# Optimization experiments

Measured on AMD Instinct MI355X. Metric: run time of the kernel, lower is better.

Reference implementation:

```python
import jax, jax.numpy as jnp
import numpy as np

D_MODEL = 1024
NUM_HEAD = 16
D_HEAD = 64
SEQ = 1024
MEM = 1024
BATCH = 4
LN_EPS = 1e-5


def _rel_shift(x):
    # x: [i, j, b, n] -- Transformer-XL relative shift trick
    i, j, b, n = x.shape
    zero_pad = jnp.zeros((i, 1, b, n), dtype=x.dtype)
    x_padded = jnp.concatenate([zero_pad, x], axis=1).reshape(j + 1, i, b, n)
    return x_padded[1:].reshape(i, j, b, n)


def setup_inputs() -> dict:
    key = jax.random.key(0)
    ks = jax.random.split(key, 8)
    w_scale = 1.0 / np.sqrt(D_MODEL)  # keep activations O(1)
    total = MEM + SEQ
    return {
        "x": jax.random.normal(ks[0], (SEQ, BATCH, D_MODEL), jnp.float32),
        "memory": jax.random.normal(ks[1], (MEM, BATCH, D_MODEL), jnp.float32),
        "pos_emb": jax.random.normal(ks[2], (total, BATCH, D_MODEL), jnp.float32),
        "pos_bias_u": jax.random.normal(ks[3], (NUM_HEAD, D_HEAD), jnp.float32) * 0.02,
        "pos_bias_v": jax.random.normal(ks[4], (NUM_HEAD, D_HEAD), jnp.float32) * 0.02,
        "W_qkv": jax.random.normal(ks[5], (3 * NUM_HEAD * D_HEAD, D_MODEL), jnp.float32) * w_scale,
        "W_rel": jax.random.normal(ks[6], (NUM_HEAD * D_HEAD, D_MODEL), jnp.float32) * w_scale,
        "W_o": jax.random.normal(ks[7], (D_MODEL, NUM_HEAD * D_HEAD), jnp.float32) * w_scale,
        "ln_gamma": jnp.ones((D_MODEL,), jnp.float32),
        "ln_beta": jnp.zeros((D_MODEL,), jnp.float32),
    }


def reference(x, memory, pos_emb, pos_bias_u, pos_bias_v, W_qkv, W_rel, W_o, ln_gamma, ln_beta):
    seq_len = x.shape[0]
    c = jnp.concatenate([memory, x], axis=0)        # [T, B, D]
    T, B = c.shape[0], c.shape[1]
    n, d = pos_bias_u.shape
    scale = 1.0 / np.sqrt(d)

    heads = c @ W_qkv.T                              # [T, B, 3*n*d]
    q, k, v = jnp.split(heads, 3, axis=-1)
    q = q.reshape(T, B, n, d)[-seq_len:]             # [S, B, n, d]
    k = k.reshape(T, B, n, d)                        # [T, B, n, d]
    v = v.reshape(T, B, n, d)
    r = (pos_emb @ W_rel.T).reshape(T, B, n, d)      # [T, B, n, d]

    AC = jnp.einsum('ibnd,jbnd->ijbn', q + pos_bias_u, k)
    BD = _rel_shift(jnp.einsum('ibnd,jbnd->ijbn', q + pos_bias_v, r))
    attn_score = (AC + BD) * scale                   # [S, T, B, n]
    attn_prob = jax.nn.softmax(attn_score, axis=1)   # softmax over key dim (dropout = eval identity)

    attn_vec = jnp.einsum('ijbn,jbnd->ibnd', attn_prob, v).reshape(seq_len, B, n * d)
    attn_out = attn_vec @ W_o.T                      # [S, B, D]

    y = x + attn_out
    mu = jnp.mean(y, axis=-1, keepdims=True)
    var = jnp.mean(jnp.square(y - mu), axis=-1, keepdims=True)
    return ln_gamma * (y - mu) / jnp.sqrt(var + LN_EPS) + ln_beta
```

## Files before the change

kernel.cpp:

```cpp
#include <hip/hip_runtime.h>

#define S_ 1024
#define M_ 1024
#define T_ 2048
#define B_ 4
#define H_ 16
#define DM_ 1024
#define DH_ 64

typedef __attribute__((ext_vector_type(8))) short s16x8;
typedef __attribute__((ext_vector_type(16))) float f32x16;

__device__ __forceinline__ unsigned short f2b(float x){
  unsigned int u = __float_as_uint(x);
  u = (u + 0x7fffu + ((u>>16)&1u)) >> 16;
  return (unsigned short)u;
}
__device__ __forceinline__ float b2f(unsigned short h){
  return __uint_as_float(((unsigned int)h)<<16);
}
__device__ __forceinline__ uint4 pack8(const float* v){
  uint4 o;
  o.x = (unsigned)f2b(v[0]) | ((unsigned)f2b(v[1])<<16);
  o.y = (unsigned)f2b(v[2]) | ((unsigned)f2b(v[3])<<16);
  o.z = (unsigned)f2b(v[4]) | ((unsigned)f2b(v[5])<<16);
  o.w = (unsigned)f2b(v[6]) | ((unsigned)f2b(v[7])<<16);
  return o;
}
__device__ __forceinline__ void glds16(const unsigned short* g, unsigned short* l){
  __builtin_amdgcn_global_load_lds((const __attribute__((address_space(1))) void*)g,
                                   (__attribute__((address_space(3))) void*)l, 16, 0, 0);
}

#define BAR_L()  asm volatile("s_waitcnt lgkmcnt(0)\ns_barrier" ::: "memory")
#define BAR_VL() asm volatile("s_waitcnt vmcnt(0) lgkmcnt(0)\ns_barrier" ::: "memory")

__global__ __launch_bounds__(256) void cast_cat(const float* __restrict__ a,
    const float* __restrict__ b, unsigned short* __restrict__ dst, int n8, int na8)
{
  int i = blockIdx.x*256 + threadIdx.x;
  if (i >= n8) return;
  const float* src = (i < na8) ? (a + (size_t)i*8) : (b + ((size_t)(i-na8))*8);
  float4 x0 = *(const float4*)src;
  float4 x1 = *(const float4*)(src+4);
  float f[8] = {x0.x,x0.y,x0.z,x0.w,x1.x,x1.y,x1.z,x1.w};
  *(uint4*)&dst[(size_t)i*8] = pack8(f);
}

__global__ __launch_bounds__(256) void gemm_nt(const unsigned short* __restrict__ A,
    const unsigned short* __restrict__ Bw, void* __restrict__ Cout,
    const float* __restrict__ res, int Ntot, int K, int mode)
{
  __shared__ __align__(16) unsigned short a_s[128*64];
  __shared__ __align__(16) unsigned short b_s[128*64];
  const int tid = threadIdx.x;
  const int lane = tid & 63, wave = tid >> 6;
  const int wr = wave >> 1, wc = wave & 1;
  const long m0 = (long)blockIdx.y * 128, n0 = (long)blockIdx.x * 128;
  f32x16 acc[2][2];
  for (int qa=0;qa<2;qa++) for(int qb=0;qb<2;qb++) for (int e=0;e<16;e++) acc[qa][qb][e]=0.f;
  int srow[4], scol[4];
  for (int c = 0; c < 4; c++) {
    int ch = c*256 + tid;
    srow[c] = ch >> 3;
    scol[c] = (((ch & 7) ^ (srow[c] & 7))) * 8;
  }
  for (int k0 = 0; k0 < K; k0 += 64) {
    for (int c = 0; c < 4; c++) {
      int ch = c*256 + tid;
      glds16(&A[(size_t)(m0+srow[c])*K + k0 + scol[c]], &a_s[ch*8]);
      glds16(&Bw[(size_t)(n0+srow[c])*K + k0 + scol[c]], &b_s[ch*8]);
    }
    __syncthreads();
    for (int ks = 0; ks < 4; ks++) {
      const int kb = ks*2 + (lane>>5);
      s16x8 af[2], bf[2];
      for (int q = 0; q < 2; q++) {
        int ra = wr*64 + q*32 + (lane&31);
        int rb = wc*64 + q*32 + (lane&31);
        af[q] = *(const s16x8*)&a_s[ra*64 + ((kb ^ (ra&7))<<3)];
        bf[q] = *(const s16x8*)&b_s[rb*64 + ((kb ^ (rb&7))<<3)];
      }
      for (int qr=0;qr<2;qr++)
        for (int qc2=0;qc2<2;qc2++)
          acc[qr][qc2] = __builtin_amdgcn_mfma_f32_32x32x16_bf16(af[qr], bf[qc2], acc[qr][qc2], 0,0,0);
    }
    __syncthreads();
  }
  for (int qr=0;qr<2;qr++)
    for (int qc2=0;qc2<2;qc2++)
      for (int e=0;e<16;e++){
        long row = m0 + wr*64 + qr*32 + (e&3) + 8*(e>>2) + 4*(lane>>5);
        long col = n0 + wc*64 + qc2*32 + (lane&31);
        size_t o = (size_t)row*Ntot + col;
        if (mode == 0) ((unsigned short*)Cout)[o] = f2b(acc[qr][qc2][e]);
        else           ((float*)Cout)[o] = acc[qr][qc2][e] + res[o];
      }
}

__global__ __launch_bounds__(256) void scatter_quv(const unsigned short* __restrict__ qkvo,
   const float* __restrict__ u, const float* __restrict__ v,
   unsigned short* __restrict__ QU, unsigned short* __restrict__ QV)
{
  int gid = blockIdx.x*256 + threadIdx.x;
  int d0 = (gid & 7) * 8;
  int i  = (gid >> 3) & (S_-1);
  int bh = gid >> 13;
  int b = bh >> 4, h = bh & 15;
  size_t src = (size_t)((M_+i)*B_ + b)*3072 + h*64 + d0;
  uint4 q8 = *(const uint4*)&qkvo[src];
  float f[8];
  f[0]=b2f(q8.x&0xffff); f[1]=b2f(q8.x>>16); f[2]=b2f(q8.y&0xffff); f[3]=b2f(q8.y>>16);
  f[4]=b2f(q8.z&0xffff); f[5]=b2f(q8.z>>16); f[6]=b2f(q8.w&0xffff); f[7]=b2f(q8.w>>16);
  float fu[8], fv[8];
  for (int e=0;e<8;e++){ fu[e] = f[e] + u[h*64+d0+e]; fv[e] = f[e] + v[h*64+d0+e]; }
  size_t dst = ((size_t)bh*S_ + i)*64 + d0;
  *(uint4*)&QU[dst] = pack8(fu);
  *(uint4*)&QV[dst] = pack8(fv);
}

__global__ __launch_bounds__(256) void scatter_vt(const unsigned short* __restrict__ qkvo,
    unsigned short* __restrict__ VT)
{
  __shared__ __align__(16) unsigned short v_s[64*72];
  const int tid = threadIdx.x;
  const int bh = blockIdx.x, b = bh>>4, h = bh&15;
  const int t0 = blockIdx.y*64;
  const unsigned short* Vg = qkvo + (size_t)b*3072 + 2048 + h*64;
  for (int c=0;c<2;c++){
    int ch = c*256 + tid;
    int r = ch>>3, off = (ch&7)*8;
    *(uint4*)&v_s[r*72+off] = *(const uint4*)&Vg[(size_t)(t0+r)*12288 + off];
  }
  __syncthreads();
  for (int c=0;c<2;c++){
    int ch = c*256 + tid;
    int d = ch>>3, toff = (ch&7)*8;
    unsigned short vals[8];
    for (int e=0;e<8;e++) vals[e] = v_s[(toff+e)*72 + d];
    uint4 pk;
    pk.x = (unsigned)vals[0] | ((unsigned)vals[1]<<16);
    pk.y = (unsigned)vals[2] | ((unsigned)vals[3]<<16);
    pk.z = (unsigned)vals[4] | ((unsigned)vals[5]<<16);
    pk.w = (unsigned)vals[6] | ((unsigned)vals[7]<<16);
    *(uint4*)&VT[((size_t)bh*64 + d)*T_ + t0 + toff] = pk;
  }
}

__global__ __launch_bounds__(256,2) void flash_attn4(
    const unsigned short* __restrict__ QU, const unsigned short* __restrict__ QV,
    const unsigned short* __restrict__ qkvo, const unsigned short* __restrict__ VT,
    const unsigned short* __restrict__ relo, unsigned short* __restrict__ AV)
{
  __shared__ __align__(16) unsigned short qu_s[64*72];
  __shared__ __align__(16) unsigned short qv_s[65*72];
  __shared__ __align__(16) unsigned short k_s [64*64];
  __shared__ __align__(16) unsigned short vt_s[2][64*64];
  __shared__ __align__(16) unsigned short rg_s[128*64];
  __shared__ __align__(16) unsigned short p_s [64*72];
  __shared__ float l_s[64];

  const int tid = threadIdx.x, lane = tid&63, wave = tid>>6;
  const int bh = blockIdx.x, b = bh>>4, h = bh&15;
  const int i0 = blockIdx.y*64;
  const int qr = wave>>1, qc = wave&1;
  const unsigned short* QUb = QU + (size_t)bh*S_*DH_;
  const unsigned short* QVb = QV + (size_t)bh*S_*DH_;
  const unsigned short* Kg  = qkvo + (size_t)b*3072 + 1024 + h*64;
  const unsigned short* VTb = VT + (size_t)bh*64*T_;
  const unsigned short* Rg  = relo + (size_t)b*1024 + h*64;

  const int s0r = tid>>3,        s0c = (((tid&7)       ^ (s0r&7)))*8;
  const int s1r = (256+tid)>>3,  s1c = ((((256+tid)&7) ^ (s1r&7)))*8;

  int vb = 0;

  glds16(&Kg [(size_t)(0+s0r)*12288 + s0c], &k_s[(size_t)tid*8]);
  glds16(&Kg [(size_t)(0+s1r)*12288 + s1c], &k_s[(size_t)(256+tid)*8]);
  glds16(&VTb[(size_t)s0r*T_ + 0 + s0c],    &vt_s[0][(size_t)tid*8]);
  glds16(&VTb[(size_t)s1r*T_ + 0 + s1c],    &vt_s[0][(size_t)(256+tid)*8]);
  {
    const int wb0 = 0 - i0 + 960;
    for (int c=0;c<4;c++){
      int ch = c*256+tid; int rr = ch>>3, off = ch&7;
      int t = wb0 + rr; t = t < 0 ? 0 : (t > T_-1 ? T_-1 : t);
      int sc = ((off ^ (rr&7)))*8;
      glds16(&Rg[(size_t)t*4096 + sc], &rg_s[(size_t)ch*8]);
    }
  }
  for (int c=0;c<2;c++){
    int ch = c*256+tid; int row = ch>>3, off=(ch&7)*8;
    *(uint4*)&qu_s[row*72+off] = *(const uint4*)&QUb[(size_t)(i0+row)*64 + off];
    *(uint4*)&qv_s[row*72+off] = *(const uint4*)&QVb[(size_t)(i0+row)*64 + off];
  }
  if (tid < 8) {
    int rr = i0 + 64; if (rr > S_-1) rr = S_-1;
    *(uint4*)&qv_s[64*72 + tid*8] = *(const uint4*)&QVb[(size_t)rr*64 + tid*8];
  }

  f32x16 acc_o;
  for (int e=0;e<16;e++) acc_o[e]=0.f;
  float lreg = 0.f;

  const int col = qc*32 + (lane&31);
  const int rbase = qr*32 + 4*(lane>>5);

  for (int j0 = 0; j0 < T_; j0 += 64) {
    const int jdmax = j0 + 63 - i0;
    const int jdmin = j0 - 63 - i0;
    const int cls = (jdmax <= 1024) ? 0 : ((jdmin >= 1026) ? 2 : 1);
    const int ashift = (cls == 2) ? 1 : 0;
    const int jn = j0 + 64;

    BAR_VL();

    if (jn < T_) {
      glds16(&VTb[(size_t)s0r*T_ + jn + s0c], &vt_s[vb^1][(size_t)tid*8]);
      glds16(&VTb[(size_t)s1r*T_ + jn + s1c], &vt_s[vb^1][(size_t)(256+tid)*8]);
    }

    f32x16 gacc0, gacc1;
    for (int e=0;e<16;e++){ gacc0[e]=0.f; gacc1[e]=0.f; }
    __builtin_amdgcn_s_setprio(1);
    for (int ks=0; ks<4; ks++){
      int koff = ks*16 + (lane>>5)*8, kb = ks*2 + (lane>>5);
      int ar = qr*32 + (lane&31) + ashift;
      s16x8 a  = *(const s16x8*)&qv_s[ar*72 + koff];
      {
        int br = (qc*2+0)*32 + (lane&31);
        s16x8 bb = *(const s16x8*)&rg_s[br*64 + ((kb ^ (br&7))<<3)];
        gacc0 = __builtin_amdgcn_mfma_f32_32x32x16_bf16(a, bb, gacc0, 0,0,0);
      }
      {
        int br = (qc*2+1)*32 + (lane&31);
        s16x8 bb = *(const s16x8*)&rg_s[br*64 + ((kb ^ (br&7))<<3)];
        gacc1 = __builtin_amdgcn_mfma_f32_32x32x16_bf16(a, bb, gacc1, 0,0,0);
      }
    }
    f32x16 acc;
    for (int e=0;e<16;e++) acc[e]=0.f;
    for (int ks=0; ks<4; ks++){
      int koff = ks*16 + (lane>>5)*8, kb = ks*2 + (lane>>5);
      int rbk = qc*32 + (lane&31);
      s16x8 a  = *(const s16x8*)&qu_s[(qr*32+(lane&31))*72 + koff];
      s16x8 bq = *(const s16x8*)&k_s[rbk*64 + ((kb ^ (rbk&7))<<3)];
      acc = __builtin_amdgcn_mfma_f32_32x32x16_bf16(a, bq, acc, 0,0,0);
    }
    __builtin_amdgcn_s_setprio(0);
    BAR_L();

    if (jn < T_) {
      glds16(&Kg[(size_t)(jn+s0r)*12288 + s0c], &k_s[(size_t)tid*8]);
      glds16(&Kg[(size_t)(jn+s1r)*12288 + s1c], &k_s[(size_t)(256+tid)*8]);
    }

    for (int e=0;e<16;e++){
      int r = rbase + (e&3) + 8*(e>>2);
      rg_s[r*128 + (qc*2+0)*32 + (lane&31)] = f2b(gacc0[e]);
      rg_s[r*128 + (qc*2+1)*32 + (lane&31)] = f2b(gacc1[e]);
    }
    BAR_L();

    for (int e=0;e<16;e++){
      int r = rbase + (e&3) + 8*(e>>2);
      int jd = j0 + col - (i0 + r);
      if (cls == 1 && jd >= 1026) continue;
      float bd = (jd == 1025) ? 0.f : b2f(rg_s[r*128 + (col - r + 63)]);
      p_s[r*72 + col] = f2b(__expf((acc[e] + bd) * 0.125f));
    }
    if (cls == 1) {
      BAR_L();
      const int wb2 = j0 - i0 - 1089;
      for (int c=0;c<4;c++){
        int ch = c*256+tid; int rr = ch>>3, off = ch&7;
        int t = wb2 + rr; t = t < 0 ? 0 : (t > T_-1 ? T_-1 : t);
        *(uint4*)&rg_s[rr*64 + ((off ^ (rr&7))<<3)] = *(const uint4*)&Rg[(size_t)t*4096 + off*8];
      }
      BAR_L();
      f32x16 g2a, g2b;
      for (int e=0;e<16;e++){ g2a[e]=0.f; g2b[e]=0.f; }
      __builtin_amdgcn_s_setprio(1);
      for (int ks=0; ks<4; ks++){
        int koff = ks*16 + (lane>>5)*8, kb = ks*2 + (lane>>5);
        int ar = qr*32 + (lane&31) + 1;
        s16x8 a  = *(const s16x8*)&qv_s[ar*72 + koff];
        {
          int br = (qc*2+0)*32 + (lane&31);
          s16x8 bb = *(const s16x8*)&rg_s[br*64 + ((kb ^ (br&7))<<3)];
          g2a = __builtin_amdgcn_mfma_f32_32x32x16_bf16(a, bb, g2a, 0,0,0);
        }
        {
          int br = (qc*2+1)*32 + (lane&31);
          s16x8 bb = *(const s16x8*)&rg_s[br*64 + ((kb ^ (br&7))<<3)];
          g2b = __builtin_amdgcn_mfma_f32_32x32x16_bf16(a, bb, g2b, 0,0,0);
        }
      }
      __builtin_amdgcn_s_setprio(0);
      BAR_L();
      for (int e=0;e<16;e++){
        int r = rbase + (e&3) + 8*(e>>2);
        rg_s[r*128 + (qc*2+0)*32 + (lane&31)] = f2b(g2a[e]);
        rg_s[r*128 + (qc*2+1)*32 + (lane&31)] = f2b(g2b[e]);
      }
      BAR_L();
      for (int e=0;e<16;e++){
        int r = rbase + (e&3) + 8*(e>>2);
        int jd = j0 + col - (i0 + r);
        if (jd < 1026) continue;
        float bd = b2f(rg_s[r*128 + (col - r + 63)]);
        p_s[r*72 + col] = f2b(__expf((acc[e] + bd) * 0.125f));
      }
    }
    BAR_L();

    if (jn < T_) {
      const int jdmaxn = jn + 63 - i0;
      const int jdminn = jn - 63 - i0;
      const int clsn = (jdmaxn <= 1024) ? 0 : ((jdminn >= 1026) ? 2 : 1);
      const int wbn = (clsn == 2) ? (jn - i0 - 1089) : (jn - i0 + 960);
      for (int c=0;c<4;c++){
        int ch = c*256+tid; int rr = ch>>3, off = ch&7;
        int t = wbn + rr; t = t < 0 ? 0 : (t > T_-1 ? T_-1 : t);
        int sc = ((off ^ (rr&7)))*8;
        glds16(&Rg[(size_t)t*4096 + sc], &rg_s[(size_t)ch*8]);
      }
    }

    {
      int rr = tid>>2, cb = (tid&3)*16;
      uint4 x0 = *(const uint4*)&p_s[rr*72+cb];
      uint4 x1 = *(const uint4*)&p_s[rr*72+cb+8];
      unsigned vs[8] = {x0.x,x0.y,x0.z,x0.w,x1.x,x1.y,x1.z,x1.w};
      float s = 0.f;
      for (int e=0;e<8;e++) s += b2f((unsigned short)(vs[e]&0xffff)) + b2f((unsigned short)(vs[e]>>16));
      s += __shfl_xor(s, 1, 64);
      s += __shfl_xor(s, 2, 64);
      if ((tid&3)==0) lreg += s;
    }
    __builtin_amdgcn_s_setprio(1);
    for (int ks=0; ks<4; ks++){
      int koff = ks*16 + (lane>>5)*8, kb = ks*2 + (lane>>5);
      int rbv = qc*32 + (lane&31);
      s16x8 a  = *(const s16x8*)&p_s[(qr*32+(lane&31))*72 + koff];
      s16x8 bv = *(const s16x8*)&vt_s[vb][rbv*64 + ((kb ^ (rbv&7))<<3)];
      acc_o = __builtin_amdgcn_mfma_f32_32x32x16_bf16(a, bv, acc_o, 0,0,0);
    }
    __builtin_amdgcn_s_setprio(0);
    vb ^= 1;
  }

  if ((tid&3)==0) l_s[tid>>2] = lreg;
  BAR_L();
  for (int e=0;e<16;e++){
    int r = rbase + (e&3) + 8*(e>>2);
    float oo = acc_o[e] / l_s[r];
    AV[ ((size_t)(i0+r)*B_ + b)*(H_*DH_) + h*DH_ + col ] = f2b(oo);
  }
}

__global__ __launch_bounds__(256) void ln_kernel(const float* __restrict__ y,
    const float* __restrict__ g, const float* __restrict__ be, float* __restrict__ o)
{
  __shared__ float red[8];
  int row = blockIdx.x, tid = threadIdx.x;
  const float* yr = y + (size_t)row*DM_;
  float v[4];
  for (int e=0;e<4;e++) v[e] = yr[tid + 256*e];
  float s = v[0]+v[1]+v[2]+v[3];
  for (int off=32; off>0; off>>=1) s += __shfl_down(s, off, 64);
  if ((tid&63)==0) red[tid>>6] = s;
  __syncthreads();
  if (tid==0) red[4] = red[0]+red[1]+red[2]+red[3];
  __syncthreads();
  float mu = red[4] * (1.f/DM_);
  __syncthreads();
  float q = 0.f;
  for (int e=0;e<4;e++){ float d = v[e]-mu; q += d*d; }
  for (int off=32; off>0; off>>=1) q += __shfl_down(q, off, 64);
  if ((tid&63)==0) red[tid>>6] = q;
  __syncthreads();
  if (tid==0) red[4] = red[0]+red[1]+red[2]+red[3];
  __syncthreads();
  float rstd = rsqrtf(red[4]*(1.f/DM_) + 1e-5f);
  for (int e=0;e<4;e++){
    int c = tid + 256*e;
    o[(size_t)row*DM_ + c] = g[c]*(v[e]-mu)*rstd + be[c];
  }
}

extern "C" void kernel_launch(void* const* d_in, const int* in_sizes, int n_in,
                              void* d_out, int out_size, void* d_ws, size_t ws_size,
                              hipStream_t stream)
{
  const float* x    = (const float*)d_in[0];
  const float* mem  = (const float*)d_in[1];
  const float* pos  = (const float*)d_in[2];
  const float* pbu  = (const float*)d_in[3];
  const float* pbv  = (const float*)d_in[4];
  const float* wqkv = (const float*)d_in[5];
  const float* wrel = (const float*)d_in[6];
  const float* wo   = (const float*)d_in[7];
  const float* gam  = (const float*)d_in[8];
  const float* bet  = (const float*)d_in[9];
  float* out = (float*)d_out;

  char* w = (char*)d_ws;
  unsigned short* qkvo  = (unsigned short*)(w + 0);
  unsigned short* relo  = (unsigned short*)(w + 50331648);
  unsigned short* wo16  = (unsigned short*)(w + 67108864);
  unsigned short* QUb   = (unsigned short*)(w + 69206016);
  unsigned short* QVb   = (unsigned short*)(w + 77594624);
  unsigned short* VT    = (unsigned short*)(w + 85983232);
  unsigned short* av16  = (unsigned short*)(w + 102760448);
  float*          yf    = (float*)(w + 111149056);
  unsigned short* c16   = (unsigned short*)(w + 127926272);
  unsigned short* pos16 = (unsigned short*)(w + 144703488);
  unsigned short* wq16  = (unsigned short*)(w + 161480704);
  unsigned short* wr16  = (unsigned short*)(w + 167772160);

  cast_cat<<<4096, 256, 0, stream>>>(mem, x, c16, 1048576, 524288);
  cast_cat<<<4096, 256, 0, stream>>>(pos, pos, pos16, 1048576, 1048576);
  cast_cat<<<1536, 256, 0, stream>>>(wqkv, wqkv, wq16, 393216, 393216);
  cast_cat<<< 512, 256, 0, stream>>>(wrel, wrel, wr16, 131072, 131072);
  cast_cat<<< 512, 256, 0, stream>>>(wo,   wo,   wo16, 131072, 131072);

  gemm_nt<<<dim3(24,64), 256, 0, stream>>>(c16,   wq16, (void*)qkvo, nullptr, 3072, 1024, 0);
  gemm_nt<<<dim3(8,64),  256, 0, stream>>>(pos16, wr16, (void*)relo, nullptr, 1024, 1024, 0);

  scatter_quv<<<2048, 256, 0, stream>>>(qkvo, pbu, pbv, QUb, QVb);
  scatter_vt<<<dim3(64,32), 256, 0, stream>>>(qkvo, VT);

  flash_attn4<<<dim3(64,16), 256, 0, stream>>>(QUb, QVb, qkvo, VT, relo, av16);

  gemm_nt<<<dim3(8,32), 256, 0, stream>>>(av16, wo16, (void*)yf, x, 1024, 1024, 1);
  ln_kernel<<<4096, 256, 0, stream>>>(yf, gam, bet, out);
}
```

Baseline: 522.5 us.

## Do rel-shift via ds_bpermute, prefetch next rel tile early, fuse cast kernels

The relative-shift of the BD scores now uses cross-lane ds_bpermute on the MFMA accumulators instead of writing them to shared memory and reading them back. This removes an LDS round trip and a barrier per tile. The rel-position tile for the next iteration is issued earlier, right after the K prefetch, using direct global-to-LDS loads, and the middle-class recompute path also switches to async loads. The five fp32-to-bf16 cast launches are merged into one kernel to cut launch overhead. The cost is more intricate lane indexing and a new ordering between the rg_s reuse and its prefetch, both of which have to stay correct.

```diff
diff --git a/kernel.cpp b/kernel.cpp
--- a/kernel.cpp
+++ b/kernel.cpp
@@ -35,16 +35,26 @@
 #define BAR_L()  asm volatile("s_waitcnt lgkmcnt(0)\ns_barrier" ::: "memory")
 #define BAR_VL() asm volatile("s_waitcnt vmcnt(0) lgkmcnt(0)\ns_barrier" ::: "memory")
 
-__global__ __launch_bounds__(256) void cast_cat(const float* __restrict__ a,
-    const float* __restrict__ b, unsigned short* __restrict__ dst, int n8, int na8)
-{
-  int i = blockIdx.x*256 + threadIdx.x;
-  if (i >= n8) return;
-  const float* src = (i < na8) ? (a + (size_t)i*8) : (b + ((size_t)(i-na8))*8);
-  float4 x0 = *(const float4*)src;
-  float4 x1 = *(const float4*)(src+4);
+__global__ __launch_bounds__(256) void cast_all(
+    const float* __restrict__ mem, const float* __restrict__ x,
+    const float* __restrict__ pos, const float* __restrict__ wqkv,
+    const float* __restrict__ wrel, const float* __restrict__ wo,
+    unsigned short* __restrict__ c16, unsigned short* __restrict__ pos16,
+    unsigned short* __restrict__ wq16, unsigned short* __restrict__ wr16,
+    unsigned short* __restrict__ wo16)
+{
+  int u = blockIdx.x*256 + threadIdx.x;
+  const float* s; unsigned short* d;
+  if (u < 1048576)      { s = (u < 524288) ? mem + (size_t)u*8 : x + (size_t)(u-524288)*8;
+                          d = c16 + (size_t)u*8; }
+  else if (u < 2097152) { int v = u - 1048576; s = pos  + (size_t)v*8; d = pos16 + (size_t)v*8; }
+  else if (u < 2490368) { int v = u - 2097152; s = wqkv + (size_t)v*8; d = wq16  + (size_t)v*8; }
+  else if (u < 2621440) { int v = u - 2490368; s = wrel + (size_t)v*8; d = wr16  + (size_t)v*8; }
+  else                  { int v = u - 2621440; s = wo   + (size_t)v*8; d = wo16  + (size_t)v*8; }
+  float4 x0 = *(const float4*)s;
+  float4 x1 = *(const float4*)(s+4);
   float f[8] = {x0.x,x0.y,x0.z,x0.w,x1.x,x1.y,x1.z,x1.w};
-  *(uint4*)&dst[(size_t)i*8] = pack8(f);
+  *(uint4*)d = pack8(f);
 }
 
 __global__ __launch_bounds__(256) void gemm_nt(const unsigned short* __restrict__ A,
@@ -164,6 +174,7 @@
   const int bh = blockIdx.x, b = bh>>4, h = bh&15;
   const int i0 = blockIdx.y*64;
   const int qr = wave>>1, qc = wave&1;
+  const int hi = lane>>5, ll = lane&31;
   const unsigned short* QUb = QU + (size_t)bh*S_*DH_;
   const unsigned short* QVb = QV + (size_t)bh*S_*DH_;
   const unsigned short* Kg  = qkvo + (size_t)b*3072 + 1024 + h*64;
@@ -202,8 +213,8 @@
   for (int e=0;e<16;e++) acc_o[e]=0.f;
   float lreg = 0.f;
 
-  const int col = qc*32 + (lane&31);
-  const int rbase = qr*32 + 4*(lane>>5);
+  const int col = qc*32 + ll;
+  const int cbase = (qc - qr + 1) * 32;
 
   for (int j0 = 0; j0 < T_; j0 += 64) {
     const int jdmax = j0 + 63 - i0;
@@ -223,16 +234,16 @@
     for (int e=0;e<16;e++){ gacc0[e]=0.f; gacc1[e]=0.f; }
     __builtin_amdgcn_s_setprio(1);
     for (int ks=0; ks<4; ks++){
-      int koff = ks*16 + (lane>>5)*8, kb = ks*2 + (lane>>5);
-      int ar = qr*32 + (lane&31) + ashift;
+      int koff = ks*16 + hi*8, kb = ks*2 + hi;
+      int ar = qr*32 + ll + ashift;
       s16x8 a  = *(const s16x8*)&qv_s[ar*72 + koff];
       {
-        int br = (qc*2+0)*32 + (lane&31);
+        int br = cbase + ll;
         s16x8 bb = *(const s16x8*)&rg_s[br*64 + ((kb ^ (br&7))<<3)];
         gacc0 = __builtin_amdgcn_mfma_f32_32x32x16_bf16(a, bb, gacc0, 0,0,0);
       }
       {
-        int br = (qc*2+1)*32 + (lane&31);
+        int br = cbase + 32 + ll;
         s16x8 bb = *(const s16x8*)&rg_s[br*64 + ((kb ^ (br&7))<<3)];
         gacc1 = __builtin_amdgcn_mfma_f32_32x32x16_bf16(a, bb, gacc1, 0,0,0);
       }
@@ -240,9 +251,9 @@
     f32x16 acc;
     for (int e=0;e<16;e++) acc[e]=0.f;
     for (int ks=0; ks<4; ks++){
-      int koff = ks*16 + (lane>>5)*8, kb = ks*2 + (lane>>5);
-      int rbk = qc*32 + (lane&31);
-      s16x8 a  = *(const s16x8*)&qu_s[(qr*32+(lane&31))*72 + koff];
+      int koff = ks*16 + hi*8, kb = ks*2 + hi;
+      int rbk = qc*32 + ll;
+      s16x8 a  = *(const s16x8*)&qu_s[(qr*32+ll)*72 + koff];
       s16x8 bq = *(const s16x8*)&k_s[rbk*64 + ((kb ^ (rbk&7))<<3)];
       acc = __builtin_amdgcn_mfma_f32_32x32x16_bf16(a, bq, acc, 0,0,0);
     }
@@ -252,78 +263,87 @@
     if (jn < T_) {
       glds16(&Kg[(size_t)(jn+s0r)*12288 + s0c], &k_s[(size_t)tid*8]);
       glds16(&Kg[(size_t)(jn+s1r)*12288 + s1c], &k_s[(size_t)(256+tid)*8]);
+      if (cls != 1) {
+        const int jdmaxn = jn + 63 - i0;
+        const int jdminn = jn - 63 - i0;
+        const int clsn = (jdmaxn <= 1024) ? 0 : ((jdminn >= 1026) ? 2 : 1);
+        const int wbn = (clsn == 2) ? (jn - i0 - 1089) : (jn - i0 + 960);
+        for (int c=0;c<4;c++){
+          int ch = c*256+tid; int rr = ch>>3, off = ch&7;
+          int t = wbn + rr; t = t < 0 ? 0 : (t > T_-1 ? T_-1 : t);
+          int sc = ((off ^ (rr&7)))*8;
+          glds16(&Rg[(size_t)t*4096 + sc], &rg_s[(size_t)ch*8]);
+        }
+      }
     }
 
     for (int e=0;e<16;e++){
-      int r = rbase + (e&3) + 8*(e>>2);
-      rg_s[r*128 + (qc*2+0)*32 + (lane&31)] = f2b(gacc0[e]);
-      rg_s[r*128 + (qc*2+1)*32 + (lane&31)] = f2b(gacc1[e]);
-    }
-    BAR_L();
-
-    for (int e=0;e<16;e++){
-      int r = rbase + (e&3) + 8*(e>>2);
+      int rm = 4*hi + (e&3) + 8*(e>>2);
+      int r  = qr*32 + rm;
       int jd = j0 + col - (i0 + r);
-      if (cls == 1 && jd >= 1026) continue;
-      float bd = (jd == 1025) ? 0.f : b2f(rg_s[r*128 + (col - r + 63)]);
-      p_s[r*72 + col] = f2b(__expf((acc[e] + bd) * 0.125f));
-    }
+      int li = ((((ll - rm + 31) & 31) | (hi<<5)) << 2);
+      float g0 = __uint_as_float((unsigned)__builtin_amdgcn_ds_bpermute(li, (int)__float_as_uint(gacc0[e])));
+      float g1 = __uint_as_float((unsigned)__builtin_amdgcn_ds_bpermute(li, (int)__float_as_uint(gacc1[e])));
+      float bd = (ll > rm) ? g1 : g0;
+      if (jd == 1025) bd = 0.f;
+      float p = __expf((acc[e] + bd) * 0.125f);
+      if (!(cls == 1 && jd >= 1026)) p_s[r*72 + col] = f2b(p);
+    }
+
     if (cls == 1) {
-      BAR_L();
       const int wb2 = j0 - i0 - 1089;
       for (int c=0;c<4;c++){
         int ch = c*256+tid; int rr = ch>>3, off = ch&7;
         int t = wb2 + rr; t = t < 0 ? 0 : (t > T_-1 ? T_-1 : t);
-        *(uint4*)&rg_s[rr*64 + ((off ^ (rr&7))<<3)] = *(const uint4*)&Rg[(size_t)t*4096 + off*8];
-      }
-      BAR_L();
+        int sc = ((off ^ (rr&7)))*8;
+        glds16(&Rg[(size_t)t*4096 + sc], &rg_s[(size_t)ch*8]);
+      }
+      BAR_VL();
       f32x16 g2a, g2b;
       for (int e=0;e<16;e++){ g2a[e]=0.f; g2b[e]=0.f; }
       __builtin_amdgcn_s_setprio(1);
       for (int ks=0; ks<4; ks++){
-        int koff = ks*16 + (lane>>5)*8, kb = ks*2 + (lane>>5);
-        int ar = qr*32 + (lane&31) + 1;
+        int koff = ks*16 + hi*8, kb = ks*2 + hi;
+        int ar = qr*32 + ll + 1;
         s16x8 a  = *(const s16x8*)&qv_s[ar*72 + koff];
         {
-          int br = (qc*2+0)*32 + (lane&31);
+          int br = cbase + ll;
           s16x8 bb = *(const s16x8*)&rg_s[br*64 + ((kb ^ (br&7))<<3)];
           g2a = __builtin_amdgcn_mfma_f32_32x32x16_bf16(a, bb, g2a, 0,0,0);
         }
         {
-          int br = (qc*2+1)*32 + (lane&31);
+          int br = cbase + 32 + ll;
           s16x8 bb = *(const s16x8*)&rg_s[br*64 + ((kb ^ (br&7))<<3)];
           g2b = __builtin_amdgcn_mfma_f32_32x32x16_bf16(a, bb, g2b, 0,0,0);
         }
       }
       __builtin_amdgcn_s_setprio(0);
+      for (int e=0;e<16;e++){
+        int rm = 4*hi + (e&3) + 8*(e>>2);
+        int r  = qr*32 + rm;
+        int jd = j0 + col - (i0 + r);
+        int li = ((((ll - rm + 31) & 31) | (hi<<5)) << 2);
+        float g0 = __uint_as_float((unsigned)__builtin_amdgcn_ds_bpermute(li, (int)__float_as_uint(g2a[e])));
+        float g1 = __uint_as_float((unsigned)__builtin_amdgcn_ds_bpermute(li, (int)__float_as_uint(g2b[e])));
+        float bd = (ll > rm) ? g1 : g0;
+        float p = __expf((acc[e] + bd) * 0.125f);
+        if (jd >= 1026) p_s[r*72 + col] = f2b(p);
+      }
       BAR_L();
-      for (int e=0;e<16;e++){
-        int r = rbase + (e&3) + 8*(e>>2);
-        rg_s[r*128 + (qc*2+0)*32 + (lane&31)] = f2b(g2a[e]);
-        rg_s[r*128 + (qc*2+1)*32 + (lane&31)] = f2b(g2b[e]);
-      }
+      if (jn < T_) {
+        const int jdmaxn = jn + 63 - i0;
+        const int jdminn = jn - 63 - i0;
+        const int clsn = (jdmaxn <= 1024) ? 0 : ((jdminn >= 1026) ? 2 : 1);
+        const int wbn = (clsn == 2) ? (jn - i0 - 1089) : (jn - i0 + 960);
+        for (int c=0;c<4;c++){
+          int ch = c*256+tid; int rr = ch>>3, off = ch&7;
+          int t = wbn + rr; t = t < 0 ? 0 : (t > T_-1 ? T_-1 : t);
+          int sc = ((off ^ (rr&7)))*8;
+          glds16(&Rg[(size_t)t*4096 + sc], &rg_s[(size_t)ch*8]);
+        }
+      }
+    } else {
       BAR_L();
-      for (int e=0;e<16;e++){
-        int r = rbase + (e&3) + 8*(e>>2);
-        int jd = j0 + col - (i0 + r);
-        if (jd < 1026) continue;
-        float bd = b2f(rg_s[r*128 + (col - r + 63)]);
-        p_s[r*72 + col] = f2b(__expf((acc[e] + bd) * 0.125f));
-      }
-    }
-    BAR_L();
-
-    if (jn < T_) {
-      const int jdmaxn = jn + 63 - i0;
-      const int jdminn = jn - 63 - i0;
-      const int clsn = (jdmaxn <= 1024) ? 0 : ((jdminn >= 1026) ? 2 : 1);
-      const int wbn = (clsn == 2) ? (jn - i0 - 1089) : (jn - i0 + 960);
-      for (int c=0;c<4;c++){
-        int ch = c*256+tid; int rr = ch>>3, off = ch&7;
-        int t = wbn + rr; t = t < 0 ? 0 : (t > T_-1 ? T_-1 : t);
-        int sc = ((off ^ (rr&7)))*8;
-        glds16(&Rg[(size_t)t*4096 + sc], &rg_s[(size_t)ch*8]);
-      }
     }
 
     {
@@ -339,9 +359,9 @@
     }
     __builtin_amdgcn_s_setprio(1);
     for (int ks=0; ks<4; ks++){
-      int koff = ks*16 + (lane>>5)*8, kb = ks*2 + (lane>>5);
-      int rbv = qc*32 + (lane&31);
-      s16x8 a  = *(const s16x8*)&p_s[(qr*32+(lane&31))*72 + koff];
+      int koff = ks*16 + hi*8, kb = ks*2 + hi;
+      int rbv = qc*32 + ll;
+      s16x8 a  = *(const s16x8*)&p_s[(qr*32+ll)*72 + koff];
       s16x8 bv = *(const s16x8*)&vt_s[vb][rbv*64 + ((kb ^ (rbv&7))<<3)];
       acc_o = __builtin_amdgcn_mfma_f32_32x32x16_bf16(a, bv, acc_o, 0,0,0);
     }
@@ -352,7 +372,7 @@
   if ((tid&3)==0) l_s[tid>>2] = lreg;
   BAR_L();
   for (int e=0;e<16;e++){
-    int r = rbase + (e&3) + 8*(e>>2);
+    int r = qr*32 + 4*hi + (e&3) + 8*(e>>2);
     float oo = acc_o[e] / l_s[r];
     AV[ ((size_t)(i0+r)*B_ + b)*(H_*DH_) + h*DH_ + col ] = f2b(oo);
   }
@@ -418,11 +438,8 @@
   unsigned short* wq16  = (unsigned short*)(w + 161480704);
   unsigned short* wr16  = (unsigned short*)(w + 167772160);
 
-  cast_cat<<<4096, 256, 0, stream>>>(mem, x, c16, 1048576, 524288);
-  cast_cat<<<4096, 256, 0, stream>>>(pos, pos, pos16, 1048576, 1048576);
-  cast_cat<<<1536, 256, 0, stream>>>(wqkv, wqkv, wq16, 393216, 393216);
-  cast_cat<<< 512, 256, 0, stream>>>(wrel, wrel, wr16, 131072, 131072);
-  cast_cat<<< 512, 256, 0, stream>>>(wo,   wo,   wo16, 131072, 131072);
+  cast_all<<<10752, 256, 0, stream>>>(mem, x, pos, wqkv, wrel, wo,
+                                      c16, pos16, wq16, wr16, wo16);
 
   gemm_nt<<<dim3(24,64), 256, 0, stream>>>(c16,   wq16, (void*)qkvo, nullptr, 3072, 1024, 0);
   gemm_nt<<<dim3(8,64),  256, 0, stream>>>(pos16, wr16, (void*)relo, nullptr, 1024, 1024, 0);
```

After: 503.9 us. 1.04x faster.
